# Kernel tuning notes

Measured on AMD Instinct MI355X. Metric: run time of the kernel, lower is better.

## Reference

```python
import jax, jax.numpy as jnp
import numpy as np
import math

# D4 group multiplication permutations (rows of the 8x8 regular representation)
PERMS = (
    (0, 1, 2, 3, 4, 5, 6, 7),
    (3, 0, 1, 2, 5, 6, 7, 4),
    (2, 3, 0, 1, 6, 7, 4, 5),
    (1, 2, 3, 0, 7, 4, 5, 6),
    (4, 5, 6, 7, 0, 1, 2, 3),
    (5, 6, 7, 4, 3, 0, 1, 2),
    (6, 7, 4, 5, 2, 3, 0, 1),
    (7, 4, 5, 6, 1, 2, 3, 0),
)


def d4_1x1(x, w):
    """D4-equivariant 1x1 conv. x: (b, cin*8, h, w), w: (cout, cin, 8)."""
    b, C, h, ww = x.shape
    cout, cin, _ = w.shape
    # (cout, 8, cin, 8): permuted copies of the base weight
    W = jnp.stack([w[..., jnp.array(p)] for p in PERMS], axis=1)
    xr = x.reshape(b, cin, 8, h, ww)
    y = jnp.einsum('ogif,bifhw->boghw', W, xr)
    return y.reshape(b, cout * 8, h, ww)


def group_norm(x, gamma, beta, num_groups, eps=1e-5):
    b, C, h, w = x.shape
    xg = x.reshape(b, num_groups, C // num_groups, h, w)
    mean = xg.mean(axis=(2, 3, 4), keepdims=True)
    var = xg.var(axis=(2, 3, 4), keepdims=True)
    xn = ((xg - mean) / jnp.sqrt(var + eps)).reshape(b, C, h, w)
    return xn * gamma[None, :, None, None] + beta[None, :, None, None]


def unfold_patches(x, k):
    """torch.nn.Unfold(k, 1, (k-1)//2, 1) -> (b, C, k*k, h, w), patch idx = ki*k+kj."""
    b, C, h, w = x.shape
    p = (k - 1) // 2
    xp = jnp.pad(x, ((0, 0), (0, 0), (p, p), (p, p)))
    pats = jnp.stack([xp[:, :, i:i + h, j:j + w]
                      for i in range(k) for j in range(k)], axis=2)
    return pats


def setup_inputs() -> dict:
    key = jax.random.key(0)
    ks = jax.random.split(key, 4)
    b, H, W = 8, 56, 56
    cin, cout, rr, k, gc = 64, 64, 2, 3, 16
    cmid = cin // rr            # 32
    G = cout // gc              # 4 dynamic-kernel groups
    x = jax.random.normal(ks[0], (b, cin * 8, H, W), jnp.float32)
    w_v = jax.random.normal(ks[1], (cout, cin, 8), jnp.float32) / math.sqrt(8 * cin / 2)
    w1 = jax.random.normal(ks[2], (cmid, cin, 8), jnp.float32) / math.sqrt(8 * cin / 2)
    gn_gamma = jnp.ones((cmid * 8,), jnp.float32)
    gn_beta = jnp.zeros((cmid * 8,), jnp.float32)
    w2 = jax.random.normal(ks[3], (k * k * G, cmid), jnp.float32) / math.sqrt(cmid)
    b2 = jnp.zeros((k * k * G,), jnp.float32)
    return {"x": x, "w_v": w_v, "w1": w1, "gn_gamma": gn_gamma,
            "gn_beta": gn_beta, "w2": w2, "b2": b2}


def reference(x, w_v, w1, gn_gamma, gn_beta, w2, b2):
    k, gc = 3, 16
    b, _, h, w = x.shape
    cmid = w1.shape[0]
    G = w2.shape[0] // (k * k)
    # --- dynamic kernel branch: conv1 (D4 1x1 + GN + ReLU), conv2 (1x1x1 conv3d)
    t = jax.nn.relu(group_norm(d4_1x1(x, w1), gn_gamma, gn_beta, cmid))
    tr = t.reshape(b, cmid, 8, h, w)
    wgt = jnp.einsum('oi,bighw->boghw', w2, tr) + b2[None, :, None, None, None]
    wv = wgt.reshape(b, G, k, k, 8, h, w)
    # --- D4 symmetrization of the k x k kernel per group element
    s = [wv[:, :, :, :, g] for g in range(8)]          # each (b,G,k,k,h,w)
    sw = [jnp.swapaxes(s[g], 2, 3) for g in range(4, 8)]
    trans = [s[0],
             jnp.rot90(s[1], 1, (2, 3)),
             jnp.rot90(s[2], 2, (2, 3)),
             jnp.rot90(s[3], 3, (2, 3)),
             jnp.rot90(sw[0], 3, (2, 3)),
             jnp.rot90(sw[1], 2, (2, 3)),
             jnp.rot90(sw[2], 1, (2, 3)),
             sw[3]]
    wv = jnp.stack(trans, axis=4)                      # (b,G,k,k,8,h,w)
    wv = wv.reshape(b, G, k * k, 8, h, w)[:, :, None]  # (b,G,1,k^2,8,h,w)
    wv = jnp.swapaxes(wv, 3, 4)                        # (b,G,1,8,k^2,h,w)
    # --- value branch + unfold + multiply-sum
    xv = d4_1x1(x, w_v)                                # (b, cout*8, h, w)
    pats = unfold_patches(xv, k).reshape(b, G, gc, 8, k * k, h, w)
    out = (wv * pats).sum(axis=4)                      # (b,G,gc,8,h,w)
    return out.reshape(b, G * gc * 8, h, w)
```

## Files before the change

### kernel.cpp

```cpp
#include <hip/hip_runtime.h>

#define BATCH 8
#define PIX   3136
#define CIN8  512
#define CMID8 256
#define KDIM  512

typedef short short8 __attribute__((ext_vector_type(8)));
typedef float f32x4 __attribute__((ext_vector_type(4)));

__constant__ int c_perms[8][8] = {
    {0, 1, 2, 3, 4, 5, 6, 7},
    {3, 0, 1, 2, 5, 6, 7, 4},
    {2, 3, 0, 1, 6, 7, 4, 5},
    {1, 2, 3, 0, 7, 4, 5, 6},
    {4, 5, 6, 7, 0, 1, 2, 3},
    {5, 6, 7, 4, 3, 0, 1, 2},
    {6, 7, 4, 5, 2, 3, 0, 1},
};
__constant__ int c_perm7[8] = {7, 4, 5, 6, 1, 2, 3, 0};

__constant__ int c_tab[8][9] = {
    {0, 1, 2, 3, 4, 5, 6, 7, 8},
    {2, 5, 8, 1, 4, 7, 0, 3, 6},
    {8, 7, 6, 5, 4, 3, 2, 1, 0},
    {6, 3, 0, 7, 4, 1, 8, 5, 2},
    {2, 1, 0, 5, 4, 3, 8, 7, 6},
    {8, 5, 2, 7, 4, 1, 6, 3, 0},
    {6, 7, 8, 3, 4, 5, 0, 1, 2},
    {0, 3, 6, 1, 4, 7, 2, 5, 8},
};

__device__ __forceinline__ float bf2f(unsigned short u) {
    union { unsigned int i; float f; } v;
    v.i = ((unsigned int)u) << 16;
    return v.f;
}
__device__ __forceinline__ unsigned short f2bf(float f) {
    union { float f; unsigned int u; } v;
    v.f = f;
    unsigned int u = v.u;
    u += 0x7FFFu + ((u >> 16) & 1u);
    return (unsigned short)(u >> 16);
}
__device__ __forceinline__ float bflo(unsigned int u) {
    union { unsigned int i; float f; } v; v.i = u << 16; return v.f;
}
__device__ __forceinline__ float bfhi(unsigned int u) {
    union { unsigned int i; float f; } v; v.i = u & 0xFFFF0000u; return v.f;
}

__device__ __forceinline__ void gload_lds16(const unsigned short* g, unsigned short* l) {
    __builtin_amdgcn_global_load_lds(
        (const __attribute__((address_space(1))) unsigned int*)g,
        (__attribute__((address_space(3))) unsigned int*)l,
        16, 0, 0);
}

#define LDT 70
__global__ __launch_bounds__(256) void cvt_t_kernel(
    const float* __restrict__ x, unsigned short* __restrict__ xbfT)
{
    __shared__ unsigned short T[64 * LDT];
    const int flat = blockIdx.x;
    const int kt = flat & 7;
    const int pt = (flat >> 3) % 49;
    const int b  = flat / (49 * 8);
    const int k0 = kt * 64, p0 = pt * 64;

    const float* xb = x + ((size_t)b * CIN8 + k0) * PIX + p0;
    const int kl = threadIdx.x >> 4;
    const int pl = (threadIdx.x & 15) * 4;
#pragma unroll
    for (int pass = 0; pass < 4; ++pass) {
        int kk = kl + pass * 16;
        float4 v = *(const float4*)(xb + (size_t)kk * PIX + pl);
        ushort2 lo = {f2bf(v.x), f2bf(v.y)};
        ushort2 hi = {f2bf(v.z), f2bf(v.w)};
        *(ushort2*)&T[kk * LDT + pl]     = lo;
        *(ushort2*)&T[kk * LDT + pl + 2] = hi;
    }
    __syncthreads();
    const int prow = threadIdx.x >> 2;
    const int kc8  = (threadIdx.x & 3) * 8;
    unsigned short* ob = xbfT + ((size_t)b * PIX + p0 + prow) * KDIM + k0;
#pragma unroll
    for (int pass = 0; pass < 2; ++pass) {
        int kk = kc8 + pass * 32;
        unsigned short tmp[8];
#pragma unroll
        for (int j = 0; j < 8; ++j) tmp[j] = T[(kk + j) * LDT + prow];
        *(uint4*)(ob + kk) = *(const uint4*)tmp;
    }
}

__global__ __launch_bounds__(256) void build_w_kernel(
    const float* __restrict__ w_v, const float* __restrict__ w1,
    unsigned short* __restrict__ Wbig, float* __restrict__ stats2)
{
    if (blockIdx.x < 2) stats2[blockIdx.x * 256 + threadIdx.x] = 0.f;

    int idx = blockIdx.x * 256 + threadIdx.x;
    int r = idx >> 9;
    int k = idx & 511;
    int i = k >> 3, f = k & 7;
    float v;
    if (r < 512) {
        int o = r >> 3, g = r & 7;
        int pf = (g < 7) ? c_perms[g][f] : c_perm7[f];
        v = w_v[(o * 64 + i) * 8 + pf];
    } else {
        int rr = r - 512;
        int o = rr >> 3, g = rr & 7;
        int pf = (g < 7) ? c_perms[g][f] : c_perm7[f];
        v = w1[(o * 64 + i) * 8 + pf];
    }
    Wbig[idx] = f2bf(v);
}

__global__ __launch_bounds__(256) void gemm_kernel(
    const unsigned short* __restrict__ xT,
    const unsigned short* __restrict__ Wbig,
    unsigned short* __restrict__ xv,
    float* __restrict__ y1,
    float* __restrict__ stats2)
{
    __shared__ unsigned short Wt[128 * 64];
    __shared__ unsigned short Xt[128 * 64];

    const int flat = blockIdx.x;
    const int rt   = flat / 196;
    const int pt   = flat - rt * 196;
    const int row0 = rt * 128;
    const int P0   = pt * 128;

    const int tid  = threadIdx.x;
    const int lane = tid & 63;
    const int wave = tid >> 6;
    const int wm   = wave & 1;
    const int wn   = wave >> 1;

    f32x4 acc[4][4];
#pragma unroll
    for (int i = 0; i < 4; ++i)
#pragma unroll
        for (int j = 0; j < 4; ++j) acc[i][j] = (f32x4){0.f, 0.f, 0.f, 0.f};

    const int lr  = lane >> 3;
    const int lc  = lane & 7;
    const int swc = ((lc ^ lr) * 8);
    const unsigned short* wsrc = Wbig + (size_t)(row0 + wave * 32 + lr) * KDIM + swc;
    const unsigned short* xsrc = xT + (size_t)(P0 + wave * 32 + lr) * KDIM + swc;
    unsigned short* wdst = &Wt[(wave * 32) * 64];
    unsigned short* xdst = &Xt[(wave * 32) * 64];

    const int m16 = lane & 15;
    const int lq  = lane >> 4;
    const int swr = m16 & 7;

    for (int kc = 0; kc < 8; ++kc) {
        const int k0 = kc * 64;
#pragma unroll
        for (int i = 0; i < 4; ++i) {
            gload_lds16(wsrc + (size_t)i * 8 * KDIM + k0, wdst + i * 512);
            gload_lds16(xsrc + (size_t)i * 8 * KDIM + k0, xdst + i * 512);
        }
        __syncthreads();

#pragma unroll
        for (int kk = 0; kk < 2; ++kk) {
            const int ck = (((kk << 2) | lq) ^ swr) * 8;
            short8 bfrag[4];
#pragma unroll
            for (int nt = 0; nt < 4; ++nt)
                bfrag[nt] = *(const short8*)&Xt[(wn * 64 + nt * 16 + m16) * 64 + ck];
#pragma unroll
            for (int mt = 0; mt < 4; ++mt) {
                short8 afrag = *(const short8*)&Wt[(wm * 64 + mt * 16 + m16) * 64 + ck];
#pragma unroll
                for (int nt = 0; nt < 4; ++nt)
                    acc[mt][nt] = __builtin_amdgcn_mfma_f32_16x16x32_bf16(
                        afrag, bfrag[nt], acc[mt][nt], 0, 0, 0);
            }
        }
        __syncthreads();
    }

    const int colw = P0 + wn * 64;
    const int bb   = colw / PIX;
    const int pq   = colw - bb * PIX;
    const int qm   = lq * 4;

    if (row0 < 512) {
        unsigned short* dst0 = xv + ((size_t)bb * CIN8) * PIX + pq + m16;
#pragma unroll
        for (int nt = 0; nt < 4; ++nt) {
            unsigned short* dst = dst0 + nt * 16;
#pragma unroll
            for (int mt = 0; mt < 4; ++mt) {
                const int m = row0 + wm * 64 + mt * 16 + qm;
#pragma unroll
                for (int r = 0; r < 4; ++r)
                    dst[(size_t)(m + r) * PIX] = f2bf(acc[mt][nt][r]);
            }
        }
    } else {
        float* dst0 = y1 + ((size_t)bb * CMID8) * PIX + pq + m16;
#pragma unroll
        for (int nt = 0; nt < 4; ++nt) {
            float* dst = dst0 + nt * 16;
#pragma unroll
            for (int mt = 0; mt < 4; ++mt) {
                const int m = (row0 - 512) + wm * 64 + mt * 16 + qm;
#pragma unroll
                for (int r = 0; r < 4; ++r)
                    dst[(size_t)(m + r) * PIX] = acc[mt][nt][r];
            }
        }
        const int gbase = ((row0 - 512) + wm * 64) >> 3;
#pragma unroll
        for (int mt = 0; mt < 4; ++mt) {
            float s = 0.f, ss = 0.f;
#pragma unroll
            for (int nt = 0; nt < 4; ++nt)
#pragma unroll
                for (int r = 0; r < 4; ++r) {
                    float v = acc[mt][nt][r];
                    s += v; ss += v * v;
                }
#pragma unroll
            for (int off = 1; off <= 16; off <<= 1) {
                s  += __shfl_xor(s, off);
                ss += __shfl_xor(ss, off);
            }
            if ((lane & 31) == 0) {
                const int g = gbase + 2 * mt + (lane >> 5);
                atomicAdd(&stats2[(bb * 32 + g) * 2],     s);
                atomicAdd(&stats2[(bb * 32 + g) * 2 + 1], ss);
            }
        }
    }
}

__global__ __launch_bounds__(256) void final_fused_kernel(
    const float* __restrict__ y1, const float* __restrict__ stats2,
    const float* __restrict__ gamma, const float* __restrict__ beta,
    const float* __restrict__ w2, const float* __restrict__ b2,
    const unsigned short* __restrict__ xv,
    float* __restrict__ out)
{
    const int combo = blockIdx.x >> 2;
    const int b    = combo >> 5;
    const int g    = (combo >> 2) & 7;
    const int gidx = combo & 3;

    __shared__ float w2s[9 * 32];
    __shared__ float b2s9[9];
    __shared__ float scs[32], shs[32];
    const int tid = threadIdx.x;
    for (int i = tid; i < 288; i += 256) {
        int tt = i >> 5, ic = i & 31;
        w2s[i] = w2[(gidx * 9 + c_tab[g][tt]) * 32 + ic];
    }
    if (tid < 9) b2s9[tid] = b2[gidx * 9 + c_tab[g][tid]];
    if (tid < 32) {
        float S  = stats2[(b * 32 + tid) * 2];
        float SS = stats2[(b * 32 + tid) * 2 + 1];
        float mean = S * (1.f / 25088.f);
        float var  = SS * (1.f / 25088.f) - mean * mean;
        float rstd = rsqrtf(var + 1e-5f);
        float sc = rstd * gamma[tid * 8 + g];
        scs[tid] = sc;
        shs[tid] = beta[tid * 8 + g] - mean * sc;
    }
    __syncthreads();

    const int pp = (blockIdx.x & 3) * 256 + tid;
    if (pp >= 784) return;
    const int p0 = pp * 4;
    const int h  = p0 / 56;
    const int w0 = p0 % 56;

    float wt[4][9];
#pragma unroll
    for (int i = 0; i < 4; ++i)
#pragma unroll
        for (int tt = 0; tt < 9; ++tt) wt[i][tt] = b2s9[tt];

    const float* yb = y1 + ((size_t)b * CMID8 + g) * PIX + p0;
#pragma unroll 4
    for (int ic = 0; ic < 32; ++ic) {
        float4 v = *(const float4*)(yb + (size_t)(ic * 8) * PIX);
        float t0 = v.x * scs[ic] + shs[ic]; t0 = t0 > 0.f ? t0 : 0.f;
        float t1 = v.y * scs[ic] + shs[ic]; t1 = t1 > 0.f ? t1 : 0.f;
        float t2 = v.z * scs[ic] + shs[ic]; t2 = t2 > 0.f ? t2 : 0.f;
        float t3 = v.w * scs[ic] + shs[ic]; t3 = t3 > 0.f ? t3 : 0.f;
#pragma unroll
        for (int tt = 0; tt < 9; ++tt) {
            float wv = w2s[tt * 32 + ic];
            wt[0][tt] = fmaf(wv, t0, wt[0][tt]);
            wt[1][tt] = fmaf(wv, t1, wt[1][tt]);
            wt[2][tt] = fmaf(wv, t2, wt[2][tt]);
            wt[3][tt] = fmaf(wv, t3, wt[3][tt]);
        }
    }

    int rb[3];
#pragma unroll
    for (int ki = 0; ki < 3; ++ki) {
        int hh = h + ki - 1;
        bool rv = (hh >= 0) & (hh < 56);
        int hc = hh < 0 ? 0 : (hh > 55 ? 55 : hh);
        rb[ki] = hc * 56;
        if (!rv) {
#pragma unroll
            for (int i = 0; i < 4; ++i)
#pragma unroll
                for (int kj = 0; kj < 3; ++kj) wt[i][ki * 3 + kj] = 0.f;
        }
    }
#pragma unroll
    for (int i = 0; i < 4; ++i)
#pragma unroll
        for (int tt = 0; tt < 9; ++tt) {
            int ww = w0 + i + (tt % 3) - 1;
            if (ww < 0 || ww >= 56) wt[i][tt] = 0.f;
        }

    const int c0 = (w0 == 0) ? 0 : (w0 - 2);

    const unsigned short* xc = xv + ((size_t)b * CIN8 + gidx * 128 + g) * PIX;
    float* ob = out + ((size_t)b * CIN8 + gidx * 128 + g) * PIX + p0;
#pragma unroll 2
    for (int cc = 0; cc < 16; ++cc) {
        f32x4 a = (f32x4){0.f, 0.f, 0.f, 0.f};
#pragma unroll
        for (int ki = 0; ki < 3; ++ki) {
            const unsigned short* row = xc + rb[ki];
            unsigned int u0 = *(const unsigned int*)(row + c0);
            unsigned int u1 = *(const unsigned int*)(row + w0);
            unsigned int u2 = *(const unsigned int*)(row + w0 + 2);
            unsigned int u3 = *(const unsigned int*)(row + w0 + 4);
            float f1 = bfhi(u0);
            float f2 = bflo(u1), f3 = bfhi(u1);
            float f4 = bflo(u2), f5 = bfhi(u2);
            float f6 = bflo(u3);
            const int t0i = ki * 3;
            a[0] = fmaf(wt[0][t0i + 0], f1, a[0]);
            a[0] = fmaf(wt[0][t0i + 1], f2, a[0]);
            a[0] = fmaf(wt[0][t0i + 2], f3, a[0]);
            a[1] = fmaf(wt[1][t0i + 0], f2, a[1]);
            a[1] = fmaf(wt[1][t0i + 1], f3, a[1]);
            a[1] = fmaf(wt[1][t0i + 2], f4, a[1]);
            a[2] = fmaf(wt[2][t0i + 0], f3, a[2]);
            a[2] = fmaf(wt[2][t0i + 1], f4, a[2]);
            a[2] = fmaf(wt[2][t0i + 2], f5, a[2]);
            a[3] = fmaf(wt[3][t0i + 0], f4, a[3]);
            a[3] = fmaf(wt[3][t0i + 1], f5, a[3]);
            a[3] = fmaf(wt[3][t0i + 2], f6, a[3]);
        }
        *(f32x4*)(ob + (size_t)cc * 8 * PIX) = a;
        xc += (size_t)8 * PIX;
    }
}

extern "C" void kernel_launch(void* const* d_in, const int* in_sizes, int n_in,
                              void* d_out, int out_size, void* d_ws, size_t ws_size,
                              hipStream_t stream) {
    (void)in_sizes; (void)n_in; (void)out_size; (void)ws_size;
    const float* x     = (const float*)d_in[0];
    const float* w_v   = (const float*)d_in[1];
    const float* w1    = (const float*)d_in[2];
    const float* gamma = (const float*)d_in[3];
    const float* beta  = (const float*)d_in[4];
    const float* w2    = (const float*)d_in[5];
    const float* b2    = (const float*)d_in[6];
    float* out = (float*)d_out;

    char* ws = (char*)d_ws;
    unsigned short* Wbig = (unsigned short*)ws;
    unsigned short* xbfT = (unsigned short*)(ws + 786432);
    unsigned short* xv   = (unsigned short*)(ws + 26476544);
    float* y1     = (float*)(ws + 52166656);
    float* stats2 = (float*)(ws + 77856768);

    cvt_t_kernel<<<3136, 256, 0, stream>>>(x, xbfT);
    build_w_kernel<<<1536, 256, 0, stream>>>(w_v, w1, Wbig, stats2);
    gemm_kernel<<<1176, 256, 0, stream>>>(xbfT, Wbig, xv, y1, stats2);
    final_fused_kernel<<<256 * 4, 256, 0, stream>>>(
        y1, stats2, gamma, beta, w2, b2, xv, out);
}
```

Before: 181.4 us.

## Double-buffer GEMM LDS tiles and swizzle block order for XCD locality

The GEMM now uses two LDS buffers, so the async global-to-LDS loads for the next K chunk are issued while MFMAs run on the current one, hiding load latency. Block indices in both the GEMM and the final fused kernel are remapped so neighbouring tiles sharing operands land on the same XCD, improving L2 reuse. The extra buffer doubles LDS use to 64KB per block, which may reduce occupancy. There is also only one barrier per iteration, so correctness relies on the trailing sync ordering writes to the other buffer.

```diff
diff --git a/kernel.cpp b/kernel.cpp
--- a/kernel.cpp
+++ b/kernel.cpp
@@ -125,12 +125,12 @@
     float* __restrict__ y1,
     float* __restrict__ stats2)
 {
-    __shared__ unsigned short Wt[128 * 64];
-    __shared__ unsigned short Xt[128 * 64];
-
-    const int flat = blockIdx.x;
-    const int rt   = flat / 196;
-    const int pt   = flat - rt * 196;
+    __shared__ unsigned short Wt[2][128 * 64];
+    __shared__ unsigned short Xt[2][128 * 64];
+
+    const int swz = (blockIdx.x & 7) * 147 + (blockIdx.x >> 3);
+    const int rt  = swz % 6;
+    const int pt  = swz / 6;
     const int row0 = rt * 128;
     const int P0   = pt * 128;
 
@@ -151,21 +151,26 @@
     const int swc = ((lc ^ lr) * 8);
     const unsigned short* wsrc = Wbig + (size_t)(row0 + wave * 32 + lr) * KDIM + swc;
     const unsigned short* xsrc = xT + (size_t)(P0 + wave * 32 + lr) * KDIM + swc;
-    unsigned short* wdst = &Wt[(wave * 32) * 64];
-    unsigned short* xdst = &Xt[(wave * 32) * 64];
+    const int wofs = (wave * 32) * 64;
 
     const int m16 = lane & 15;
     const int lq  = lane >> 4;
     const int swr = m16 & 7;
 
+#define STAGE(buf, k0) do {                                                   \
+    _Pragma("unroll")                                                         \
+    for (int i = 0; i < 4; ++i) {                                             \
+        gload_lds16(wsrc + (size_t)i * 8 * KDIM + (k0), &Wt[buf][wofs] + i * 512); \
+        gload_lds16(xsrc + (size_t)i * 8 * KDIM + (k0), &Xt[buf][wofs] + i * 512); \
+    }                                                                         \
+} while (0)
+
+    STAGE(0, 0);
+    __syncthreads();
+
+    int cur = 0;
     for (int kc = 0; kc < 8; ++kc) {
-        const int k0 = kc * 64;
-#pragma unroll
-        for (int i = 0; i < 4; ++i) {
-            gload_lds16(wsrc + (size_t)i * 8 * KDIM + k0, wdst + i * 512);
-            gload_lds16(xsrc + (size_t)i * 8 * KDIM + k0, xdst + i * 512);
-        }
-        __syncthreads();
+        if (kc < 7) STAGE(cur ^ 1, (kc + 1) * 64);
 
 #pragma unroll
         for (int kk = 0; kk < 2; ++kk) {
@@ -173,10 +178,10 @@
             short8 bfrag[4];
 #pragma unroll
             for (int nt = 0; nt < 4; ++nt)
-                bfrag[nt] = *(const short8*)&Xt[(wn * 64 + nt * 16 + m16) * 64 + ck];
+                bfrag[nt] = *(const short8*)&Xt[cur][(wn * 64 + nt * 16 + m16) * 64 + ck];
 #pragma unroll
             for (int mt = 0; mt < 4; ++mt) {
-                short8 afrag = *(const short8*)&Wt[(wm * 64 + mt * 16 + m16) * 64 + ck];
+                short8 afrag = *(const short8*)&Wt[cur][(wm * 64 + mt * 16 + m16) * 64 + ck];
 #pragma unroll
                 for (int nt = 0; nt < 4; ++nt)
                     acc[mt][nt] = __builtin_amdgcn_mfma_f32_16x16x32_bf16(
@@ -184,7 +189,9 @@
             }
         }
         __syncthreads();
-    }
+        cur ^= 1;
+    }
+#undef STAGE
 
     const int colw = P0 + wn * 64;
     const int bb   = colw / PIX;
@@ -249,7 +256,8 @@
     const unsigned short* __restrict__ xv,
     float* __restrict__ out)
 {
-    const int combo = blockIdx.x >> 2;
+    const int swz  = (blockIdx.x & 7) * 128 + (blockIdx.x >> 3);
+    const int combo = swz >> 2;
     const int b    = combo >> 5;
     const int g    = (combo >> 2) & 7;
     const int gidx = combo & 3;
@@ -275,7 +283,7 @@
     }
     __syncthreads();
 
-    const int pp = (blockIdx.x & 3) * 256 + tid;
+    const int pp = (swz & 3) * 256 + tid;
     if (pp >= 784) return;
     const int p0 = pp * 4;
     const int h  = p0 / 56;
```

Result: faster. 171.6 us (-5.4%).
